# Performance work log

Measured on AMD Instinct MI355X. Metric: run time of the kernel, lower is better.

The kernel has to match this reference:

```python
import jax, jax.numpy as jnp
import numpy as np

D_MODEL = 1024
N_HEADS = 16
WINDOW = 64              # window_size
HEAD_DIM = D_MODEL // N_HEADS
HALF = WINDOW // 2
NWIN = WINDOW + 1        # half tokens each side + self
LN_EPS = 1e-5


def _layernorm(x, g, b):
    mu = jnp.mean(x, axis=-1, keepdims=True)
    var = jnp.var(x, axis=-1, keepdims=True)
    return (x - mu) * jax.lax.rsqrt(var + LN_EPS) * g + b


def _linear_attention(q, k, v):
    # feature map phi(x) = elu(x) + 1; O(n) attention over full d_model
    q = jax.nn.elu(q) + 1.0
    k = jax.nn.elu(k) + 1.0
    kv = jnp.einsum('bsd,bse->bde', k, v)          # [B, D, D]
    num = jnp.einsum('bsd,bde->bse', q, kv)        # [B, S, D]
    denom = jnp.einsum('bsd,bd->bs', q, k.sum(axis=1))
    return num / (denom[..., None] + 1e-6)


def _window_attention(q, k, v, rel_bias):
    # sliding window attention with relative position bias, banded via offset scan
    B, S, _ = q.shape
    qh = q.reshape(B, S, N_HEADS, HEAD_DIM).transpose(0, 2, 1, 3)  # [B,H,S,Dh]
    kh = k.reshape(B, S, N_HEADS, HEAD_DIM).transpose(0, 2, 1, 3)
    vh = v.reshape(B, S, N_HEADS, HEAD_DIM).transpose(0, 2, 1, 3)
    kp = jnp.pad(kh, ((0, 0), (0, 0), (HALF, HALF), (0, 0)))
    vp = jnp.pad(vh, ((0, 0), (0, 0), (HALF, HALF), (0, 0)))
    pos = jnp.arange(S)
    scale = np.float32(1.0 / np.sqrt(HEAD_DIM))

    def score_step(_, w):
        off = w - HALF                                   # relative offset in [-HALF, HALF]
        ks = jax.lax.dynamic_slice_in_dim(kp, w, S, axis=2)   # k at position i+off
        s = jnp.einsum('bhsd,bhsd->bhs', qh, ks) * scale
        s = s + rel_bias[off + WINDOW][None, :, None]    # bias per head for this offset
        valid = (pos + off >= 0) & (pos + off < S)
        s = jnp.where(valid[None, None, :], s, -jnp.inf)
        return None, s

    _, scores = jax.lax.scan(score_step, None, jnp.arange(NWIN))  # [W,B,H,S]
    attn = jax.nn.softmax(scores, axis=0)                          # softmax over window

    def out_step(acc, aw):
        a, w = aw
        vs = jax.lax.dynamic_slice_in_dim(vp, w, S, axis=2)
        return acc + a[..., None] * vs, None

    out, _ = jax.lax.scan(out_step, jnp.zeros_like(qh), (attn, jnp.arange(NWIN)))
    return out.transpose(0, 2, 1, 3).reshape(B, S, D_MODEL)


def setup_inputs() -> dict:
    key = jax.random.key(0)
    ks = jax.random.split(key, 16)

    def lin(k, fan_in, shape):
        return (jax.random.normal(k, shape, jnp.float32) / np.sqrt(fan_in)).astype(jnp.float32)

    D = D_MODEL
    inp = {
        'x': jax.random.normal(ks[0], (2, 2048, D), jnp.float32),
        'wq_lin': lin(ks[1], D, (D, D)), 'bq_lin': jnp.zeros((D,), jnp.float32),
        'wk_lin': lin(ks[2], D, (D, D)), 'bk_lin': jnp.zeros((D,), jnp.float32),
        'wv_lin': lin(ks[3], D, (D, D)), 'bv_lin': jnp.zeros((D,), jnp.float32),
        'wq_loc': lin(ks[4], D, (D, D)), 'bq_loc': jnp.zeros((D,), jnp.float32),
        'wk_loc': lin(ks[5], D, (D, D)), 'bk_loc': jnp.zeros((D,), jnp.float32),
        'wv_loc': lin(ks[6], D, (D, D)), 'bv_loc': jnp.zeros((D,), jnp.float32),
        'wo': lin(ks[7], D, (D, D)), 'bo': jnp.zeros((D,), jnp.float32),
        'wg1': lin(ks[8], 3 * D, (3 * D, D)), 'bg1': jnp.zeros((D,), jnp.float32),
        'wg2': lin(ks[9], D, (D, D)), 'bg2': jnp.zeros((D,), jnp.float32),
        'rel_bias': jax.random.normal(ks[10], (2 * WINDOW + 1, N_HEADS), jnp.float32),
        'ln_g': jnp.ones((D,), jnp.float32),
        'ln_b': jnp.zeros((D,), jnp.float32),
    }
    return inp


def reference(x, wq_lin, bq_lin, wk_lin, bk_lin, wv_lin, bv_lin,
              wq_loc, bq_loc, wk_loc, bk_loc, wv_loc, bv_loc,
              wo, bo, wg1, bg1, wg2, bg2, rel_bias, ln_g, ln_b):
    h = _layernorm(x, ln_g, ln_b)
    lin_out = _linear_attention(h @ wq_lin + bq_lin,
                                h @ wk_lin + bk_lin,
                                h @ wv_lin + bv_lin)
    win_out = _window_attention(h @ wq_loc + bq_loc,
                                h @ wk_loc + bk_loc,
                                h @ wv_loc + bv_loc, rel_bias)
    gate_in = jnp.concatenate([lin_out, win_out, h], axis=-1)
    gate = jax.nn.sigmoid(jnp.maximum(gate_in @ wg1 + bg1, 0.0) @ wg2 + bg2)
    out = gate * lin_out + (1.0 - gate) * win_out
    return out @ wo + bo + x
```

## Files before the change

kernel.cpp:

```cpp
#include <hip/hip_runtime.h>

typedef unsigned short u16;
typedef unsigned int u32;
typedef float f32x4 __attribute__((ext_vector_type(4)));
typedef __bf16 bf16x8 __attribute__((ext_vector_type(8)));

#define SEQ 2048
#define DM 1024

__device__ __forceinline__ float bf2f(u16 a){
  u32 b = ((u32)a) << 16; float f; __builtin_memcpy(&f, &b, 4); return f;
}
__device__ __forceinline__ u16 f2bf(float f){
  u32 b; __builtin_memcpy(&b, &f, 4);
  b += 0x7fffu + ((b >> 16) & 1u);
  return (u16)(b >> 16);
}

__device__ __forceinline__ void gload16(const void* g, void* l){
  __builtin_amdgcn_global_load_lds((const __attribute__((address_space(1))) u32*)g,
                                   (__attribute__((address_space(3))) u32*)l, 16, 0, 0);
}

#define SBAR  __builtin_amdgcn_sched_barrier(0); __builtin_amdgcn_s_barrier(); __builtin_amdgcn_sched_barrier(0);
#define VM0   asm volatile("s_waitcnt vmcnt(0)" ::: "memory"); __builtin_amdgcn_sched_barrier(0);
#define VM6   asm volatile("s_waitcnt vmcnt(6)" ::: "memory"); __builtin_amdgcn_sched_barrier(0);
#define VM8   asm volatile("s_waitcnt vmcnt(8)" ::: "memory"); __builtin_amdgcn_sched_barrier(0);

#define MFMA16(AF, BF) \
  __builtin_amdgcn_s_setprio(1); \
  _Pragma("unroll") for (int m_ = 0; m_ < 4; m_++) \
  _Pragma("unroll") for (int n_ = 0; n_ < 4; n_++) \
    acc[m_][n_] = __builtin_amdgcn_mfma_f32_16x16x32_bf16(AF[m_], BF[n_], acc[m_][n_], 0,0,0); \
  __builtin_amdgcn_s_setprio(0);

struct TP { const float* src[9]; u16* dst[9]; int K[9]; };

__global__ __launch_bounds__(256) void ktransall(TP tp){
  __shared__ float tile[64][65];
  int z = blockIdx.z;
  int K = tp.K[z];
  int kb = blockIdx.y << 6, nb = blockIdx.x << 6;
  if (kb >= K) return;
  const float* W = tp.src[z];
  u16* WT = tp.dst[z];
  const int N = 1024;
  int t = threadIdx.x;
  #pragma unroll
  for (int i = 0; i < 4; i++){
    int idx = t + (i << 8);
    int r = idx >> 4, c = (idx & 15) << 2;
    float4 v = *(const float4*)(W + (size_t)(kb + r) * N + nb + c);
    tile[r][c] = v.x; tile[r][c+1] = v.y; tile[r][c+2] = v.z; tile[r][c+3] = v.w;
  }
  __syncthreads();
  #pragma unroll
  for (int i = 0; i < 2; i++){
    int idx = t + (i << 8);
    int n = idx >> 3, k8 = (idx & 7) << 3;
    union { u16 s[8]; int4 v; } u;
    #pragma unroll
    for (int j = 0; j < 8; j++) u.s[j] = f2bf(tile[k8 + j][n]);
    *(int4*)(WT + (size_t)(nb + n) * K + kb + k8) = u.v;
  }
}

__global__ __launch_bounds__(256) void kln(const float* __restrict__ x, const float* __restrict__ gg,
                                           const float* __restrict__ bb, u16* __restrict__ h){
  int row = blockIdx.x, t = threadIdx.x;
  float4 xv = ((const float4*)(x + (size_t)row * DM))[t];
  float s  = xv.x + xv.y + xv.z + xv.w;
  float s2 = xv.x*xv.x + xv.y*xv.y + xv.z*xv.z + xv.w*xv.w;
  #pragma unroll
  for (int o = 1; o < 64; o <<= 1){ s += __shfl_xor(s, o); s2 += __shfl_xor(s2, o); }
  __shared__ float r1[4], r2[4];
  if ((t & 63) == 0){ r1[t >> 6] = s; r2[t >> 6] = s2; }
  __syncthreads();
  float S = r1[0]+r1[1]+r1[2]+r1[3], S2 = r2[0]+r2[1]+r2[2]+r2[3];
  float mu = S * (1.0f/DM);
  float var = S2 * (1.0f/DM) - mu*mu;
  float rstd = rsqrtf(var + 1e-5f);
  float4 gv = ((const float4*)gg)[t], bv = ((const float4*)bb)[t];
  ushort4 o;
  o.x = f2bf((xv.x - mu)*rstd*gv.x + bv.x);
  o.y = f2bf((xv.y - mu)*rstd*gv.y + bv.y);
  o.z = f2bf((xv.z - mu)*rstd*gv.z + bv.z);
  o.w = f2bf((xv.w - mu)*rstd*gv.w + bv.w);
  ((ushort4*)(h + (size_t)row * DM))[t] = o;
}

__device__ __forceinline__ float phi_elu(float v){ return v > 0.f ? v + 1.f : __expf(v); }

__global__ __launch_bounds__(512, 2) void kqkv8(
  const u16* __restrict__ h,
  const u16* wt0, const u16* wt1, const u16* wt2, const u16* wt3, const u16* wt4, const u16* wt5,
  const float* b0, const float* b1, const float* b2, const float* b3, const float* b4, const float* b5,
  u16* phiQ, u16* phiKT, u16* vT, u16* qloc, u16* kloc, u16* vloc)
{
  extern __shared__ char smem[];
  char* LA0 = smem;
  char* LA1 = smem + 16384;
  char* LB0 = smem + 32768;
  char* LB1 = smem + 65536;

  const int t = threadIdx.x, lane = t & 63, w = t >> 6;
  const int wm = w >> 2, wn = w & 3;

  int bid = blockIdx.x;
  int swz = (bid & 7) * 96 + (bid >> 3);
  int mt = swz & 31, ntile = swz >> 5;
  int m0 = mt << 7;
  int n0g = ntile << 8;
  int wi = n0g >> 10;
  int n0 = n0g & 1023;
  const u16* Bp = wi==0?wt0: wi==1?wt1: wi==2?wt2: wi==3?wt3: wi==4?wt4: wt5;
  const float* bsel = wi==0?b0: wi==1?b1: wi==2?b2: wi==3?b3: wi==4?b4: b5;

  auto stageA = [&](char* dst, int kt){
    #pragma unroll
    for (int j = 0; j < 2; j++){
      int slot = (j << 9) + t;
      int r = slot >> 3;
      int csw = ((slot & 7) << 4) ^ ((r & 7) << 4);
      gload16((const char*)(h + (size_t)(m0 + r) * 1024 + (kt << 6)) + csw,
              dst + (((j << 9) + (w << 6)) << 4));
    }
  };
  auto stageB = [&](char* dst, int kt){
    #pragma unroll
    for (int j = 0; j < 4; j++){
      int slot = (j << 9) + t;
      int r = slot >> 3;
      int csw = ((slot & 7) << 4) ^ ((r & 7) << 4);
      gload16((const char*)(Bp + (size_t)(n0 + r) * 1024 + (kt << 6)) + csw,
              dst + (((j << 9) + (w << 6)) << 4));
    }
  };
  auto rdA = [&](const char* ab, int m, int kk) -> bf16x8 {
    int ra = (wm << 6) + (m << 4) + (lane & 15);
    return *(const bf16x8*)(ab + (ra << 7) + (((kk << 6) + ((lane >> 4) << 4)) ^ ((ra & 7) << 4)));
  };
  auto rdB = [&](const char* bb, int n, int kk) -> bf16x8 {
    int rb = (wn << 6) + (n << 4) + (lane & 15);
    return *(const bf16x8*)(bb + (rb << 7) + (((kk << 6) + ((lane >> 4) << 4)) ^ ((rb & 7) << 4)));
  };

  f32x4 acc[4][4];
  #pragma unroll
  for (int m = 0; m < 4; m++)
    #pragma unroll
    for (int n = 0; n < 4; n++) acc[m][n] = (f32x4){0.f,0.f,0.f,0.f};

  const int NT = 16;
  bf16x8 a0[4], bq0[4], a1[4], bq1[4];

  stageA(LA0, 0); stageB(LB0, 0);
  stageA(LA1, 1); stageB(LB1, 1);
  VM6 SBAR
  #pragma unroll
  for (int m = 0; m < 4; m++) a0[m] = rdA(LA0, m, 0);
  #pragma unroll
  for (int n = 0; n < 4; n++) bq0[n] = rdB(LB0, n, 0);

  #pragma unroll 1
  for (int i = 0; i < NT/2; i++){
    int e = 2*i, o = e + 1;
    int se = (e + 2 < NT) ? e + 2 : NT - 1;
    int so = (o + 2 < NT) ? o + 2 : NT - 1;
    #pragma unroll
    for (int m = 0; m < 4; m++) a1[m] = rdA(LA0, m, 1);
    #pragma unroll
    for (int n = 0; n < 4; n++) bq1[n] = rdB(LB0, n, 1);
    SBAR
    stageA(LA0, se); stageB(LB0, se);
    MFMA16(a0, bq0)
    VM6 SBAR
    #pragma unroll
    for (int m = 0; m < 4; m++) a0[m] = rdA(LA1, m, 0);
    #pragma unroll
    for (int n = 0; n < 4; n++) bq0[n] = rdB(LB1, n, 0);
    MFMA16(a1, bq1)
    #pragma unroll
    for (int m = 0; m < 4; m++) a1[m] = rdA(LA1, m, 1);
    #pragma unroll
    for (int n = 0; n < 4; n++) bq1[n] = rdB(LB1, n, 1);
    SBAR
    stageA(LA1, so); stageB(LB1, so);
    MFMA16(a0, bq0)
    VM6 SBAR
    if (i < NT/2 - 1){
      #pragma unroll
      for (int m = 0; m < 4; m++) a0[m] = rdA(LA0, m, 0);
      #pragma unroll
      for (int n = 0; n < 4; n++) bq0[n] = rdB(LB0, n, 0);
    }
    MFMA16(a1, bq1)
  }
  VM0

  #pragma unroll
  for (int n = 0; n < 4; n++){
    int col = n0 + (wn << 6) + (n << 4) + (lane & 15);
    float bv = bsel[col];
    #pragma unroll
    for (int m = 0; m < 4; m++){
      int r0 = m0 + (wm << 6) + (m << 4) + ((lane >> 4) << 2);
      float e[4];
      #pragma unroll
      for (int r = 0; r < 4; r++) e[r] = acc[m][n][r] + bv;
      if (wi == 0){
        #pragma unroll
        for (int r = 0; r < 4; r++) phiQ[(size_t)(r0 + r) * DM + col] = f2bf(phi_elu(e[r]));
      } else if (wi == 1 || wi == 2){
        union { u16 s[4]; ushort4 v; } o;
        #pragma unroll
        for (int r = 0; r < 4; r++) o.s[r] = f2bf(wi == 1 ? phi_elu(e[r]) : e[r]);
        int bb = r0 >> 11, sl = r0 & 2047;
        u16* dst = (wi == 1) ? phiKT : vT;
        *(ushort4*)(dst + ((size_t)(bb << 10) + col) * SEQ + sl) = o.v;
      } else {
        u16* dst = wi==3 ? qloc : wi==4 ? kloc : vloc;
        #pragma unroll
        for (int r = 0; r < 4; r++) dst[(size_t)(r0 + r) * DM + col] = f2bf(e[r]);
      }
    }
  }
}

template<int NCHUNK>
__device__ __forceinline__ void pipe128(const u16* A0c, const u16* A1c, const u16* A2c, int lda,
                                        const u16* B, int ldb, int K, int m0, int n0,
                                        char* LA0, char* LA1, char* LB0, char* LB1,
                                        f32x4 (&acc)[4][4])
{
  const int t = threadIdx.x, lane = t & 63, w = t >> 6;
  const int wm = w >> 1, wn = w & 1;
  const int NT = K >> 6;

  auto stageA = [&](char* dst, int kt){
    const u16* Ab;
    if (NCHUNK == 3){
      int ci = kt >> 4;
      const u16* cp = (ci == 0) ? A0c : ((ci == 1) ? A1c : A2c);
      Ab = cp + ((kt & 15) << 6);
    } else {
      Ab = A0c + (kt << 6);
    }
    #pragma unroll
    for (int j = 0; j < 4; j++){
      int slot = (j << 8) + t;
      int r = slot >> 3;
      int csw = ((slot & 7) << 4) ^ ((r & 7) << 4);
// ... 48 lines not shown
    for (int m = 0; m < 4; m++) a0[m] = rdA(LA1, m, 0);
    #pragma unroll
    for (int n = 0; n < 4; n++) bq0[n] = rdB(LB1, n, 0);
    MFMA16(a1, bq1)
    #pragma unroll
    for (int m = 0; m < 4; m++) a1[m] = rdA(LA1, m, 1);
    #pragma unroll
    for (int n = 0; n < 4; n++) bq1[n] = rdB(LB1, n, 1);
    SBAR
    stageA(LA1, so); stageB(LB1, so);
    MFMA16(a0, bq0)
    VM8 SBAR
    if (i < NT/2 - 1){
      #pragma unroll
      for (int m = 0; m < 4; m++) a0[m] = rdA(LA0, m, 0);
      #pragma unroll
      for (int n = 0; n < 4; n++) bq0[n] = rdB(LB0, n, 0);
    }
    MFMA16(a1, bq1)
  }
  VM0
}

#define PIPE_LDS \
  __shared__ char LA0[16384], LA1[16384], LB0[16384], LB1[16384];

#define EPI_COORDS \
  const int lane = threadIdx.x & 63, w = threadIdx.x >> 6; \
  const int wm = w >> 1, wn = w & 1;

#define ZERO_ACC f32x4 acc[4][4]; \
  _Pragma("unroll") for (int m = 0; m < 4; m++) _Pragma("unroll") for (int n = 0; n < 4; n++) acc[m][n] = (f32x4){0.f,0.f,0.f,0.f};

__global__ __launch_bounds__(256) void kkv(const u16* __restrict__ vT, const u16* __restrict__ phiKT,
                                           u16* __restrict__ kvT){
  PIPE_LDS
  int b = blockIdx.z;
  int m0 = blockIdx.x << 7, n0 = blockIdx.y << 7;
  const u16* A = vT + (size_t)b * DM * SEQ;
  const u16* B = phiKT + (size_t)b * DM * SEQ;
  ZERO_ACC
  pipe128<1>(A, 0, 0, SEQ, B, SEQ, SEQ, m0, n0, LA0, LA1, LB0, LB1, acc);
  EPI_COORDS
  u16* C = kvT + (size_t)b * DM * DM;
  #pragma unroll
  for (int n = 0; n < 4; n++){
    int col = n0 + wn*64 + n*16 + (lane & 15);
    #pragma unroll
    for (int m = 0; m < 4; m++){
      int r0 = m0 + wm*64 + m*16 + ((lane >> 4) << 2);
      #pragma unroll
      for (int r = 0; r < 4; r++) C[(size_t)(r0 + r) * DM + col] = f2bf(acc[m][n][r]);
    }
  }
}

__global__ __launch_bounds__(256) void knum(const u16* __restrict__ phiQ, const u16* __restrict__ kvT,
                                            const float* __restrict__ dn, u16* __restrict__ lin){
  PIPE_LDS
  int b = blockIdx.z;
  int m0 = blockIdx.x << 7, n0 = blockIdx.y << 7;
  const u16* A = phiQ + (size_t)b * SEQ * DM;
  const u16* B = kvT + (size_t)b * DM * DM;
  ZERO_ACC
  pipe128<1>(A, 0, 0, DM, B, DM, DM, m0, n0, LA0, LA1, LB0, LB1, acc);
  EPI_COORDS
  #pragma unroll
  for (int n = 0; n < 4; n++){
    int col = n0 + wn*64 + n*16 + (lane & 15);
    #pragma unroll
    for (int m = 0; m < 4; m++){
      int r0 = m0 + wm*64 + m*16 + ((lane >> 4) << 2);
      #pragma unroll
      for (int r = 0; r < 4; r++){
        float d = dn[(b << 11) + r0 + r] + 1e-6f;
        lin[((size_t)(b << 11) + r0 + r) * DM + col] = f2bf(acc[m][n][r] / d);
      }
    }
  }
}

__global__ __launch_bounds__(256) void ksumk(const u16* __restrict__ kt, float* __restrict__ ks){
  int row = blockIdx.x, t = threadIdx.x;
  const ushort4* src = (const ushort4*)(kt + (size_t)row * SEQ);
  float s = 0.f;
  for (int i = t; i < 512; i += 256){
    ushort4 v = src[i];
    s += bf2f(v.x) + bf2f(v.y) + bf2f(v.z) + bf2f(v.w);
  }
  #pragma unroll
  for (int o = 1; o < 64; o <<= 1) s += __shfl_xor(s, o);
  __shared__ float red[4];
  if ((t & 63) == 0) red[t >> 6] = s;
  __syncthreads();
  if (t == 0) ks[row] = red[0] + red[1] + red[2] + red[3];
}

__global__ __launch_bounds__(256) void kdenom(const u16* __restrict__ phiQ, const float* __restrict__ ks,
                                              float* __restrict__ dn){
  int row = blockIdx.x, t = threadIdx.x;
  ushort4 v = ((const ushort4*)(phiQ + (size_t)row * DM))[t];
  float4 kk = ((const float4*)(ks + ((size_t)(row >> 11) << 10)))[t];
  float s = bf2f(v.x)*kk.x + bf2f(v.y)*kk.y + bf2f(v.z)*kk.z + bf2f(v.w)*kk.w;
  #pragma unroll
  for (int o = 1; o < 64; o <<= 1) s += __shfl_xor(s, o);
  __shared__ float red[4];
  if ((t & 63) == 0) red[t >> 6] = s;
  __syncthreads();
  if (t == 0) dn[row] = red[0] + red[1] + red[2] + red[3];
}

__global__ __launch_bounds__(256) void kwin(const u16* __restrict__ qloc, const u16* __restrict__ kloc,
                                            const u16* __restrict__ vloc, const float* __restrict__ rel_bias,
                                            u16* __restrict__ wout)
{
  __shared__ float KV[128 * 68];
  __shared__ float Ssm[64 * 84];
  __shared__ float bias_s[65];
  int qt = blockIdx.x, hh = blockIdx.y, b = blockIdx.z;
  int q0 = qt << 6;
  int t = threadIdx.x;
  int q = t >> 2, sub = t & 3, qq = q & 15;
  size_t base = (size_t)b * SEQ * DM + hh * 64;
  for (int i = t; i < 1024; i += 256){
    int r = i >> 3, seg = i & 7;
    int p = q0 + r - 32;
    float* dst = &KV[r * 68 + (seg << 3)];
    if ((unsigned)p < SEQ){
      int4 raw = *(const int4*)(kloc + base + (size_t)p * DM + (seg << 3));
      const u16* s = (const u16*)&raw;
      #pragma unroll
      for (int j = 0; j < 8; j++) dst[j] = bf2f(s[j]);
    } else {
      #pragma unroll
      for (int j = 0; j < 8; j++) dst[j] = 0.f;
    }
  }
  if (t < 65) bias_s[t] = rel_bias[(t + 32) * 16 + hh];
  float qreg[16];
  {
    const u16* qp = qloc + base + (size_t)(q0 + q) * DM + (sub << 4);
    int4 raw0 = *(const int4*)qp;
    int4 raw1 = *(const int4*)(qp + 8);
    const u16* s0 = (const u16*)&raw0; const u16* s1 = (const u16*)&raw1;
    #pragma unroll
    for (int j = 0; j < 8; j++){ qreg[j] = bf2f(s0[j]); qreg[8 + j] = bf2f(s1[j]); }
  }
  __syncthreads();
  int rlo = (t >> 6) << 4;
  for (int rr = 0; rr < 80; rr++){
    int r = rlo + rr;
    const float* kr = &KV[r * 68 + (sub << 4)];
    float s = 0.f;
    #pragma unroll
    for (int i = 0; i < 16; i++) s += qreg[i] * kr[i];
    s += __shfl_xor(s, 1); s += __shfl_xor(s, 2);
    int wrel = r - q;
    int p = q0 + r - 32;
    float sc = -1e30f;
    if ((unsigned)wrel <= 64u && (unsigned)p < SEQ) sc = s * 0.125f + bias_s[wrel];
    if (sub == 0) Ssm[q * 84 + rr] = sc;
  }
  __syncthreads();
  for (int i = t; i < 1024; i += 256){
    int r = i >> 3, seg = i & 7;
    int p = q0 + r - 32;
    float* dst = &KV[r * 68 + (seg << 3)];
    if ((unsigned)p < SEQ){
      int4 raw = *(const int4*)(vloc + base + (size_t)p * DM + (seg << 3));
      const u16* s = (const u16*)&raw;
      #pragma unroll
      for (int j = 0; j < 8; j++) dst[j] = bf2f(s[j]);
    } else {
      #pragma unroll
      for (int j = 0; j < 8; j++) dst[j] = 0.f;
    }
  }
  float mloc = -1e30f;
  for (int wrel = sub; wrel <= 64; wrel += 4) mloc = fmaxf(mloc, Ssm[q * 84 + qq + wrel]);
  mloc = fmaxf(mloc, __shfl_xor(mloc, 1));
  mloc = fmaxf(mloc, __shfl_xor(mloc, 2));
  float lloc = 0.f;
  for (int wrel = sub; wrel <= 64; wrel += 4) lloc += __expf(Ssm[q * 84 + qq + wrel] - mloc);
  lloc += __shfl_xor(lloc, 1); lloc += __shfl_xor(lloc, 2);
  float inv = 1.0f / lloc;
  for (int wrel = sub; wrel <= 64; wrel += 4)
    Ssm[q * 84 + qq + wrel] = __expf(Ssm[q * 84 + qq + wrel] - mloc) * inv;
  __syncthreads();
  float accv[16];
  #pragma unroll
  for (int i = 0; i < 16; i++) accv[i] = 0.f;
  for (int rr = 0; rr < 80; rr++){
    int r = rlo + rr;
    float pv = Ssm[q * 84 + rr];
    pv = ((unsigned)(r - q) <= 64u) ? pv : 0.f;
    const float* vr = &KV[r * 68 + (sub << 4)];
    #pragma unroll
    for (int i = 0; i < 16; i++) accv[i] += pv * vr[i];
  }
  union { u16 s[16]; int4 v[2]; } ob;
  #pragma unroll
  for (int i = 0; i < 16; i++) ob.s[i] = f2bf(accv[i]);
  u16* dst = wout + base + (size_t)(q0 + q) * DM + (sub << 4);
  *(int4*)dst = ob.v[0];
  *(int4*)(dst + 8) = ob.v[1];
}

__global__ __launch_bounds__(256) void kgate1(const u16* __restrict__ lin, const u16* __restrict__ win,
                                              const u16* __restrict__ h, const u16* __restrict__ wg1T,
                                              const float* __restrict__ bg1, u16* __restrict__ g1){
  PIPE_LDS
  int m0 = blockIdx.x << 7, n0 = blockIdx.y << 7;
  ZERO_ACC
  pipe128<3>(lin, win, h, DM, wg1T, 3072, 3072, m0, n0, LA0, LA1, LB0, LB1, acc);
  EPI_COORDS
  #pragma unroll
  for (int n = 0; n < 4; n++){
    int col = n0 + wn*64 + n*16 + (lane & 15);
    float bv = bg1[col];
    #pragma unroll
    for (int m = 0; m < 4; m++){
      int r0 = m0 + wm*64 + m*16 + ((lane >> 4) << 2);
      #pragma unroll
      for (int r = 0; r < 4; r++){
        float v = acc[m][n][r] + bv;
        g1[(size_t)(r0 + r) * DM + col] = f2bf(v > 0.f ? v : 0.f);
      }
    }
  }
}

__global__ __launch_bounds__(256) void kgate2(const u16* __restrict__ g1, const u16* __restrict__ wg2T,
                                              const float* __restrict__ bg2, const u16* __restrict__ lin,
                                              const u16* __restrict__ win, u16* __restrict__ outc){
  PIPE_LDS
  int m0 = blockIdx.x << 7, n0 = blockIdx.y << 7;
  ZERO_ACC
  pipe128<1>(g1, 0, 0, DM, wg2T, DM, DM, m0, n0, LA0, LA1, LB0, LB1, acc);
// ... 48 lines not shown
  const float* wq_lin = (const float*)d_in[1];  const float* bq_lin = (const float*)d_in[2];
  const float* wk_lin = (const float*)d_in[3];  const float* bk_lin = (const float*)d_in[4];
  const float* wv_lin = (const float*)d_in[5];  const float* bv_lin = (const float*)d_in[6];
  const float* wq_loc = (const float*)d_in[7];  const float* bq_loc = (const float*)d_in[8];
  const float* wk_loc = (const float*)d_in[9];  const float* bk_loc = (const float*)d_in[10];
  const float* wv_loc = (const float*)d_in[11]; const float* bv_loc = (const float*)d_in[12];
  const float* wo     = (const float*)d_in[13]; const float* bo     = (const float*)d_in[14];
  const float* wg1    = (const float*)d_in[15]; const float* bg1    = (const float*)d_in[16];
  const float* wg2    = (const float*)d_in[17]; const float* bg2    = (const float*)d_in[18];
  const float* rel_bias = (const float*)d_in[19];
  const float* ln_g   = (const float*)d_in[20]; const float* ln_b   = (const float*)d_in[21];

  char* ws = (char*)d_ws;
  size_t off = 0;
  auto alloc = [&](size_t bytes) -> void* {
    void* p = ws + off;
    off += (bytes + 255) & ~(size_t)255;
    return p;
  };
  const size_t MB2 = (size_t)1024 * 1024 * 2;
  const size_t ACT = (size_t)4096 * 1024 * 2;
  u16* wT[6]; for (int i = 0; i < 6; i++) wT[i] = (u16*)alloc(MB2);
  u16* woT   = (u16*)alloc(MB2);
  u16* wg1T  = (u16*)alloc((size_t)1024 * 3072 * 2);
  u16* wg2T  = (u16*)alloc(MB2);
  u16* hbf   = (u16*)alloc(ACT);
  u16* phiQ  = (u16*)alloc(ACT);
  u16* phiKT = (u16*)alloc(ACT);
  u16* vT    = (u16*)alloc(ACT);
  u16* qloc  = (u16*)alloc(ACT);
  u16* kloc  = (u16*)alloc(ACT);
  u16* vloc  = (u16*)alloc(ACT);
  u16* kvT   = (u16*)alloc(2 * MB2);
  float* ksum = (float*)alloc(2 * 1024 * 4);
  float* dnm  = (float*)alloc(4096 * 4);
  u16* lin   = (u16*)alloc(ACT);
  u16* win   = (u16*)alloc(ACT);
  u16* g1    = phiQ;
  u16* outc  = vT;

  hipFuncSetAttribute((const void*)kqkv8, hipFuncAttributeMaxDynamicSharedMemorySize, 98304);

  dim3 blk(256);
  TP tp;
  tp.src[0]=wq_lin; tp.src[1]=wk_lin; tp.src[2]=wv_lin; tp.src[3]=wq_loc; tp.src[4]=wk_loc;
  tp.src[5]=wv_loc; tp.src[6]=wo; tp.src[7]=wg1; tp.src[8]=wg2;
  tp.dst[0]=wT[0]; tp.dst[1]=wT[1]; tp.dst[2]=wT[2]; tp.dst[3]=wT[3]; tp.dst[4]=wT[4];
  tp.dst[5]=wT[5]; tp.dst[6]=woT; tp.dst[7]=wg1T; tp.dst[8]=wg2T;
  for (int i = 0; i < 9; i++) tp.K[i] = (i == 7) ? 3072 : 1024;
  ktransall<<<dim3(16,48,9), blk, 0, stream>>>(tp);

  kln<<<4096, blk, 0, stream>>>(x, ln_g, ln_b, hbf);

  kqkv8<<<768, 512, 98304, stream>>>(hbf, wT[0], wT[1], wT[2], wT[3], wT[4], wT[5],
                                     bq_lin, bk_lin, bv_lin, bq_loc, bk_loc, bv_loc,
                                     phiQ, phiKT, vT, qloc, kloc, vloc);

  ksumk<<<2048, blk, 0, stream>>>(phiKT, ksum);
  kdenom<<<4096, blk, 0, stream>>>(phiQ, ksum, dnm);
  kkv<<<dim3(8,8,2), blk, 0, stream>>>(vT, phiKT, kvT);
  knum<<<dim3(16,8,2), blk, 0, stream>>>(phiQ, kvT, dnm, lin);

  kwin<<<dim3(32,16,2), blk, 0, stream>>>(qloc, kloc, vloc, rel_bias, win);

  kgate1<<<dim3(32,8), blk, 0, stream>>>(lin, win, hbf, wg1T, bg1, g1);
  kgate2<<<dim3(32,8), blk, 0, stream>>>(g1, wg2T, bg2, lin, win, outc);
  kfinal<<<dim3(32,8), blk, 0, stream>>>(outc, woT, bo, x, (float*)d_out);
}
```

Before: 264.4 us.

## Enlarge QKV projection GEMM tile to 256x256 with 4 waves per block

The fused six-way QKV projection kernel moves from 128x256 tiles with 8 waves (2 blocks per CU) to 256x256 tiles with 4 waves, each wave computing a 128x128 sub-tile with an 8x8 MFMA accumulator grid. The aim is more operand reuse per LDS read and less global traffic per FLOP. The cost is heavy register pressure from 64 accumulator vectors plus fragments, only one block per CU, 128 KB of LDS, and just 384 blocks on the GPU. The wait counts are updated to match the larger number of loads per stage.

```diff
diff --git a/kernel.cpp b/kernel.cpp
--- a/kernel.cpp
+++ b/kernel.cpp
@@ -24,13 +24,20 @@
 
 #define SBAR  __builtin_amdgcn_sched_barrier(0); __builtin_amdgcn_s_barrier(); __builtin_amdgcn_sched_barrier(0);
 #define VM0   asm volatile("s_waitcnt vmcnt(0)" ::: "memory"); __builtin_amdgcn_sched_barrier(0);
-#define VM6   asm volatile("s_waitcnt vmcnt(6)" ::: "memory"); __builtin_amdgcn_sched_barrier(0);
 #define VM8   asm volatile("s_waitcnt vmcnt(8)" ::: "memory"); __builtin_amdgcn_sched_barrier(0);
+#define VM16  asm volatile("s_waitcnt vmcnt(16)" ::: "memory"); __builtin_amdgcn_sched_barrier(0);
 
 #define MFMA16(AF, BF) \
   __builtin_amdgcn_s_setprio(1); \
   _Pragma("unroll") for (int m_ = 0; m_ < 4; m_++) \
   _Pragma("unroll") for (int n_ = 0; n_ < 4; n_++) \
+    acc[m_][n_] = __builtin_amdgcn_mfma_f32_16x16x32_bf16(AF[m_], BF[n_], acc[m_][n_], 0,0,0); \
+  __builtin_amdgcn_s_setprio(0);
+
+#define MFMA64(AF, BF) \
+  __builtin_amdgcn_s_setprio(1); \
+  _Pragma("unroll") for (int m_ = 0; m_ < 8; m_++) \
+  _Pragma("unroll") for (int n_ = 0; n_ < 8; n_++) \
     acc[m_][n_] = __builtin_amdgcn_mfma_f32_16x16x32_bf16(AF[m_], BF[n_], acc[m_][n_], 0,0,0); \
   __builtin_amdgcn_s_setprio(0);
 
@@ -91,7 +98,7 @@
 
 __device__ __forceinline__ float phi_elu(float v){ return v > 0.f ? v + 1.f : __expf(v); }
 
-__global__ __launch_bounds__(512, 2) void kqkv8(
+__global__ __launch_bounds__(256, 1) void kqkvF(
   const u16* __restrict__ h,
   const u16* wt0, const u16* wt1, const u16* wt2, const u16* wt3, const u16* wt4, const u16* wt5,
   const float* b0, const float* b1, const float* b2, const float* b3, const float* b4, const float* b5,
@@ -99,17 +106,17 @@
 {
   extern __shared__ char smem[];
   char* LA0 = smem;
-  char* LA1 = smem + 16384;
-  char* LB0 = smem + 32768;
-  char* LB1 = smem + 65536;
+  char* LA1 = smem + 32768;
+  char* LB0 = smem + 65536;
+  char* LB1 = smem + 98304;
 
   const int t = threadIdx.x, lane = t & 63, w = t >> 6;
-  const int wm = w >> 2, wn = w & 3;
+  const int wm = w >> 1, wn = w & 1;
 
   int bid = blockIdx.x;
-  int swz = (bid & 7) * 96 + (bid >> 3);
-  int mt = swz & 31, ntile = swz >> 5;
-  int m0 = mt << 7;
+  int swz = (bid & 7) * 48 + (bid >> 3);
+  int mt = swz & 15, ntile = swz >> 4;
+  int m0 = mt << 8;
   int n0g = ntile << 8;
   int wi = n0g >> 10;
   int n0 = n0g & 1023;
@@ -118,93 +125,92 @@
 
   auto stageA = [&](char* dst, int kt){
     #pragma unroll
-    for (int j = 0; j < 2; j++){
-      int slot = (j << 9) + t;
+    for (int j = 0; j < 8; j++){
+      int slot = (j << 8) + t;
       int r = slot >> 3;
       int csw = ((slot & 7) << 4) ^ ((r & 7) << 4);
       gload16((const char*)(h + (size_t)(m0 + r) * 1024 + (kt << 6)) + csw,
-              dst + (((j << 9) + (w << 6)) << 4));
+              dst + (((j << 8) + (w << 6)) << 4));
     }
   };
   auto stageB = [&](char* dst, int kt){
     #pragma unroll
-    for (int j = 0; j < 4; j++){
-      int slot = (j << 9) + t;
+    for (int j = 0; j < 8; j++){
+      int slot = (j << 8) + t;
       int r = slot >> 3;
       int csw = ((slot & 7) << 4) ^ ((r & 7) << 4);
       gload16((const char*)(Bp + (size_t)(n0 + r) * 1024 + (kt << 6)) + csw,
-              dst + (((j << 9) + (w << 6)) << 4));
+              dst + (((j << 8) + (w << 6)) << 4));
     }
   };
   auto rdA = [&](const char* ab, int m, int kk) -> bf16x8 {
-    int ra = (wm << 6) + (m << 4) + (lane & 15);
+    int ra = (wm << 7) + (m << 4) + (lane & 15);
     return *(const bf16x8*)(ab + (ra << 7) + (((kk << 6) + ((lane >> 4) << 4)) ^ ((ra & 7) << 4)));
   };
   auto rdB = [&](const char* bb, int n, int kk) -> bf16x8 {
-    int rb = (wn << 6) + (n << 4) + (lane & 15);
+    int rb = (wn << 7) + (n << 4) + (lane & 15);
     return *(const bf16x8*)(bb + (rb << 7) + (((kk << 6) + ((lane >> 4) << 4)) ^ ((rb & 7) << 4)));
   };
 
-  f32x4 acc[4][4];
-  #pragma unroll
-  for (int m = 0; m < 4; m++)
-    #pragma unroll
-    for (int n = 0; n < 4; n++) acc[m][n] = (f32x4){0.f,0.f,0.f,0.f};
-
-  const int NT = 16;
-  bf16x8 a0[4], bq0[4], a1[4], bq1[4];
+  f32x4 acc[8][8];
+  #pragma unroll
+  for (int m = 0; m < 8; m++)
+    #pragma unroll
+    for (int n = 0; n < 8; n++) acc[m][n] = (f32x4){0.f,0.f,0.f,0.f};
+
+  bf16x8 a0[8], b0f[8], a1[8], b1f[8];
 
   stageA(LA0, 0); stageB(LB0, 0);
   stageA(LA1, 1); stageB(LB1, 1);
-  VM6 SBAR
-  #pragma unroll
-  for (int m = 0; m < 4; m++) a0[m] = rdA(LA0, m, 0);
-  #pragma unroll
-  for (int n = 0; n < 4; n++) bq0[n] = rdB(LB0, n, 0);
+  VM16 SBAR
+  #pragma unroll
+  for (int m = 0; m < 8; m++) a0[m] = rdA(LA0, m, 0);
+  #pragma unroll
+  for (int n = 0; n < 8; n++) b0f[n] = rdB(LB0, n, 0);
 
   #pragma unroll 1
-  for (int i = 0; i < NT/2; i++){
+  for (int i = 0; i < 8; i++){
     int e = 2*i, o = e + 1;
-    int se = (e + 2 < NT) ? e + 2 : NT - 1;
-    int so = (o + 2 < NT) ? o + 2 : NT - 1;
-    #pragma unroll
-    for (int m = 0; m < 4; m++) a1[m] = rdA(LA0, m, 1);
-    #pragma unroll
-    for (int n = 0; n < 4; n++) bq1[n] = rdB(LB0, n, 1);
+    int se = (e + 2 < 16) ? e + 2 : 15;
+    int so = (o + 2 < 16) ? o + 2 : 15;
+    #pragma unroll
+    for (int m = 0; m < 8; m++) a1[m] = rdA(LA0, m, 1);
+    #pragma unroll
+    for (int n = 0; n < 8; n++) b1f[n] = rdB(LB0, n, 1);
     SBAR
     stageA(LA0, se); stageB(LB0, se);
-    MFMA16(a0, bq0)
-    VM6 SBAR
-    #pragma unroll
-    for (int m = 0; m < 4; m++) a0[m] = rdA(LA1, m, 0);
-    #pragma unroll
-    for (int n = 0; n < 4; n++) bq0[n] = rdB(LB1, n, 0);
-    MFMA16(a1, bq1)
-    #pragma unroll
-    for (int m = 0; m < 4; m++) a1[m] = rdA(LA1, m, 1);
-    #pragma unroll
-    for (int n = 0; n < 4; n++) bq1[n] = rdB(LB1, n, 1);
+    MFMA64(a0, b0f)
+    VM16 SBAR
+    #pragma unroll
+    for (int m = 0; m < 8; m++) a0[m] = rdA(LA1, m, 0);
+    #pragma unroll
+    for (int n = 0; n < 8; n++) b0f[n] = rdB(LB1, n, 0);
+    MFMA64(a1, b1f)
+    #pragma unroll
+    for (int m = 0; m < 8; m++) a1[m] = rdA(LA1, m, 1);
+    #pragma unroll
+    for (int n = 0; n < 8; n++) b1f[n] = rdB(LB1, n, 1);
     SBAR
     stageA(LA1, so); stageB(LB1, so);
-    MFMA16(a0, bq0)
-    VM6 SBAR
-    if (i < NT/2 - 1){
-      #pragma unroll
-      for (int m = 0; m < 4; m++) a0[m] = rdA(LA0, m, 0);
-      #pragma unroll
-      for (int n = 0; n < 4; n++) bq0[n] = rdB(LB0, n, 0);
-    }
-    MFMA16(a1, bq1)
+    MFMA64(a0, b0f)
+    VM16 SBAR
+    if (i < 7){
+      #pragma unroll
+      for (int m = 0; m < 8; m++) a0[m] = rdA(LA0, m, 0);
+      #pragma unroll
+      for (int n = 0; n < 8; n++) b0f[n] = rdB(LB0, n, 0);
+    }
+    MFMA64(a1, b1f)
   }
   VM0
 
   #pragma unroll
-  for (int n = 0; n < 4; n++){
-    int col = n0 + (wn << 6) + (n << 4) + (lane & 15);
+  for (int n = 0; n < 8; n++){
+    int col = n0 + (wn << 7) + (n << 4) + (lane & 15);
     float bv = bsel[col];
     #pragma unroll
-    for (int m = 0; m < 4; m++){
-      int r0 = m0 + (wm << 6) + (m << 4) + ((lane >> 4) << 2);
+    for (int m = 0; m < 8; m++){
+      int r0 = m0 + (wm << 7) + (m << 4) + ((lane >> 4) << 2);
       float e[4];
       #pragma unroll
       for (int r = 0; r < 4; r++) e[r] = acc[m][n][r] + bv;
@@ -212,12 +218,12 @@
         #pragma unroll
         for (int r = 0; r < 4; r++) phiQ[(size_t)(r0 + r) * DM + col] = f2bf(phi_elu(e[r]));
       } else if (wi == 1 || wi == 2){
-        union { u16 s[4]; ushort4 v; } o;
+        union { u16 s[4]; ushort4 v; } ov;
         #pragma unroll
-        for (int r = 0; r < 4; r++) o.s[r] = f2bf(wi == 1 ? phi_elu(e[r]) : e[r]);
+        for (int r = 0; r < 4; r++) ov.s[r] = f2bf(wi == 1 ? phi_elu(e[r]) : e[r]);
         int bb = r0 >> 11, sl = r0 & 2047;
         u16* dst = (wi == 1) ? phiKT : vT;
-        *(ushort4*)(dst + ((size_t)(bb << 10) + col) * SEQ + sl) = o.v;
+        *(ushort4*)(dst + ((size_t)(bb << 10) + col) * SEQ + sl) = ov.v;
       } else {
         u16* dst = wi==3 ? qloc : wi==4 ? kloc : vloc;
         #pragma unroll
@@ -625,7 +631,7 @@
   u16* g1    = phiQ;
   u16* outc  = vT;
 
-  hipFuncSetAttribute((const void*)kqkv8, hipFuncAttributeMaxDynamicSharedMemorySize, 98304);
+  hipFuncSetAttribute((const void*)kqkvF, hipFuncAttributeMaxDynamicSharedMemorySize, 131072);
 
   dim3 blk(256);
   TP tp;
@@ -638,9 +644,9 @@
 
   kln<<<4096, blk, 0, stream>>>(x, ln_g, ln_b, hbf);
 
-  kqkv8<<<768, 512, 98304, stream>>>(hbf, wT[0], wT[1], wT[2], wT[3], wT[4], wT[5],
-                                     bq_lin, bk_lin, bv_lin, bq_loc, bk_loc, bv_loc,
-                                     phiQ, phiKT, vT, qloc, kloc, vloc);
+  kqkvF<<<384, 256, 131072, stream>>>(hbf, wT[0], wT[1], wT[2], wT[3], wT[4], wT[5],
+                                      bq_lin, bk_lin, bv_lin, bq_loc, bk_loc, bv_loc,
+                                      phiQ, phiKT, vT, qloc, kloc, vloc);
 
   ksumk<<<2048, blk, 0, stream>>>(phiKT, ksum);
   kdenom<<<4096, blk, 0, stream>>>(phiQ, ksum, dnm);
```

Result: slower. 470.3 us (+77.9%).

## Switch QKV GEMM to triple-buffered LDS pipeline with simpler per-tile loop

Applied to the files above, without the earlier changes.

Restructures the fused QKV projection GEMM from a double-buffered, 2x-unrolled software pipeline with register-level fragment prefetch to a triple-buffered LDS ring (48KB per stage, 144KB total). Each iteration loads fragments, issues the prefetch two tiles ahead, and waits on LDS before each MFMA group. The aim is more latency tolerance for global loads. The cost is that the block now uses 144KB of LDS and launch bounds drop to one block per CU, which lowers occupancy and removes the overlap of LDS reads with MFMAs that the old code had.

```diff
diff --git a/kernel.cpp b/kernel.cpp
--- a/kernel.cpp
+++ b/kernel.cpp
@@ -23,6 +23,7 @@
 }
 
 #define SBAR  __builtin_amdgcn_sched_barrier(0); __builtin_amdgcn_s_barrier(); __builtin_amdgcn_sched_barrier(0);
+#define LGKM0 asm volatile("s_waitcnt lgkmcnt(0)" ::: "memory"); __builtin_amdgcn_sched_barrier(0);
 #define VM0   asm volatile("s_waitcnt vmcnt(0)" ::: "memory"); __builtin_amdgcn_sched_barrier(0);
 #define VM6   asm volatile("s_waitcnt vmcnt(6)" ::: "memory"); __builtin_amdgcn_sched_barrier(0);
 #define VM8   asm volatile("s_waitcnt vmcnt(8)" ::: "memory"); __builtin_amdgcn_sched_barrier(0);
@@ -91,18 +92,13 @@
 
 __device__ __forceinline__ float phi_elu(float v){ return v > 0.f ? v + 1.f : __expf(v); }
 
-__global__ __launch_bounds__(512, 2) void kqkv8(
+__global__ __launch_bounds__(512, 1) void kqkv9(
   const u16* __restrict__ h,
   const u16* wt0, const u16* wt1, const u16* wt2, const u16* wt3, const u16* wt4, const u16* wt5,
   const float* b0, const float* b1, const float* b2, const float* b3, const float* b4, const float* b5,
   u16* phiQ, u16* phiKT, u16* vT, u16* qloc, u16* kloc, u16* vloc)
 {
   extern __shared__ char smem[];
-  char* LA0 = smem;
-  char* LA1 = smem + 16384;
-  char* LB0 = smem + 32768;
-  char* LB1 = smem + 65536;
-
   const int t = threadIdx.x, lane = t & 63, w = t >> 6;
   const int wm = w >> 2, wn = w & 3;
 
@@ -136,11 +132,18 @@
               dst + (((j << 9) + (w << 6)) << 4));
     }
   };
-  auto rdA = [&](const char* ab, int m, int kk) -> bf16x8 {
+  auto stageTile = [&](int buf, int kt){
+    char* base = smem + buf * 49152;
+    stageA(base, kt);
+    stageB(base + 16384, kt);
+  };
+  auto rdA = [&](int buf, int m, int kk) -> bf16x8 {
+    const char* ab = smem + buf * 49152;
     int ra = (wm << 6) + (m << 4) + (lane & 15);
     return *(const bf16x8*)(ab + (ra << 7) + (((kk << 6) + ((lane >> 4) << 4)) ^ ((ra & 7) << 4)));
   };
-  auto rdB = [&](const char* bb, int n, int kk) -> bf16x8 {
+  auto rdB = [&](int buf, int n, int kk) -> bf16x8 {
+    const char* bb = smem + buf * 49152 + 16384;
     int rb = (wn << 6) + (n << 4) + (lane & 15);
     return *(const bf16x8*)(bb + (rb << 7) + (((kk << 6) + ((lane >> 4) << 4)) ^ ((rb & 7) << 4)));
   };
@@ -152,49 +155,33 @@
     for (int n = 0; n < 4; n++) acc[m][n] = (f32x4){0.f,0.f,0.f,0.f};
 
   const int NT = 16;
-  bf16x8 a0[4], bq0[4], a1[4], bq1[4];
-
-  stageA(LA0, 0); stageB(LB0, 0);
-  stageA(LA1, 1); stageB(LB1, 1);
-  VM6 SBAR
-  #pragma unroll
-  for (int m = 0; m < 4; m++) a0[m] = rdA(LA0, m, 0);
-  #pragma unroll
-  for (int n = 0; n < 4; n++) bq0[n] = rdB(LB0, n, 0);
+  stageTile(0, 0);
+  stageTile(1, 1);
+  VM6
+  SBAR
 
   #pragma unroll 1
-  for (int i = 0; i < NT/2; i++){
-    int e = 2*i, o = e + 1;
-    int se = (e + 2 < NT) ? e + 2 : NT - 1;
-    int so = (o + 2 < NT) ? o + 2 : NT - 1;
-    #pragma unroll
-    for (int m = 0; m < 4; m++) a1[m] = rdA(LA0, m, 1);
-    #pragma unroll
-    for (int n = 0; n < 4; n++) bq1[n] = rdB(LB0, n, 1);
+  for (int tt = 0; tt < NT; tt++){
+    int buf = tt % 3;
+    int st = (tt + 2 < NT) ? tt + 2 : NT - 1;
+    int sbuf = (tt + 2) % 3;
+    bf16x8 af[4], bf[4];
+    #pragma unroll
+    for (int m = 0; m < 4; m++) af[m] = rdA(buf, m, 0);
+    #pragma unroll
+    for (int n = 0; n < 4; n++) bf[n] = rdB(buf, n, 0);
     SBAR
-    stageA(LA0, se); stageB(LB0, se);
-    MFMA16(a0, bq0)
-    VM6 SBAR
-    #pragma unroll
-    for (int m = 0; m < 4; m++) a0[m] = rdA(LA1, m, 0);
-    #pragma unroll
-    for (int n = 0; n < 4; n++) bq0[n] = rdB(LB1, n, 0);
-    MFMA16(a1, bq1)
-    #pragma unroll
-    for (int m = 0; m < 4; m++) a1[m] = rdA(LA1, m, 1);
-    #pragma unroll
-    for (int n = 0; n < 4; n++) bq1[n] = rdB(LB1, n, 1);
+    stageTile(sbuf, st);
+    LGKM0
+    MFMA16(af, bf)
+    #pragma unroll
+    for (int m = 0; m < 4; m++) af[m] = rdA(buf, m, 1);
+    #pragma unroll
+    for (int n = 0; n < 4; n++) bf[n] = rdB(buf, n, 1);
+    VM6
     SBAR
-    stageA(LA1, so); stageB(LB1, so);
-    MFMA16(a0, bq0)
-    VM6 SBAR
-    if (i < NT/2 - 1){
-      #pragma unroll
-      for (int m = 0; m < 4; m++) a0[m] = rdA(LA0, m, 0);
-      #pragma unroll
-      for (int n = 0; n < 4; n++) bq0[n] = rdB(LB0, n, 0);
-    }
-    MFMA16(a1, bq1)
+    LGKM0
+    MFMA16(af, bf)
   }
   VM0
 
@@ -625,7 +612,7 @@
   u16* g1    = phiQ;
   u16* outc  = vT;
 
-  hipFuncSetAttribute((const void*)kqkv8, hipFuncAttributeMaxDynamicSharedMemorySize, 98304);
+  hipFuncSetAttribute((const void*)kqkv9, hipFuncAttributeMaxDynamicSharedMemorySize, 147456);
 
   dim3 blk(256);
   TP tp;
@@ -638,9 +625,9 @@
 
   kln<<<4096, blk, 0, stream>>>(x, ln_g, ln_b, hbf);
 
-  kqkv8<<<768, 512, 98304, stream>>>(hbf, wT[0], wT[1], wT[2], wT[3], wT[4], wT[5],
-                                     bq_lin, bk_lin, bv_lin, bq_loc, bk_loc, bv_loc,
-                                     phiQ, phiKT, vT, qloc, kloc, vloc);
+  kqkv9<<<768, 512, 147456, stream>>>(hbf, wT[0], wT[1], wT[2], wT[3], wT[4], wT[5],
+                                      bq_lin, bk_lin, bv_lin, bq_loc, bk_loc, bv_loc,
+                                      phiQ, phiKT, vT, qloc, kloc, vloc);
 
   ksumk<<<2048, blk, 0, stream>>>(phiKT, ksum);
   kdenom<<<4096, blk, 0, stream>>>(phiQ, ksum, dnm);
```

Result: no change. 265.1 us (+0.3%).

## Fuse split-K kv GEMM with window attention into one launch

Applied to the files above, without the earlier changes.

The kv GEMM is split along the sequence dimension into two halves, giving 256 tiles instead of 128. It is merged with the window-attention kernel into a single heterogeneous launch, with block index choosing the role and shared memory dynamic, so the two independent workloads share the GPU. A small kernel then sums the two bf16 partial kv products. This aims to fix underutilisation of the 128-block kv GEMM and remove launch serialisation. In exchange it adds an extra pass over the partials and rounds each partial to bf16 before summing.

```diff
diff --git a/kernel.cpp b/kernel.cpp
--- a/kernel.cpp
+++ b/kernel.cpp
@@ -332,27 +332,140 @@
 #define ZERO_ACC f32x4 acc[4][4]; \
   _Pragma("unroll") for (int m = 0; m < 4; m++) _Pragma("unroll") for (int n = 0; n < 4; n++) acc[m][n] = (f32x4){0.f,0.f,0.f,0.f};
 
-__global__ __launch_bounds__(256) void kkv(const u16* __restrict__ vT, const u16* __restrict__ phiKT,
-                                           u16* __restrict__ kvT){
-  PIPE_LDS
-  int b = blockIdx.z;
-  int m0 = blockIdx.x << 7, n0 = blockIdx.y << 7;
-  const u16* A = vT + (size_t)b * DM * SEQ;
-  const u16* B = phiKT + (size_t)b * DM * SEQ;
-  ZERO_ACC
-  pipe128<1>(A, 0, 0, SEQ, B, SEQ, SEQ, m0, n0, LA0, LA1, LB0, LB1, acc);
-  EPI_COORDS
-  u16* C = kvT + (size_t)b * DM * DM;
-  #pragma unroll
-  for (int n = 0; n < 4; n++){
-    int col = n0 + wn*64 + n*16 + (lane & 15);
-    #pragma unroll
-    for (int m = 0; m < 4; m++){
-      int r0 = m0 + wm*64 + m*16 + ((lane >> 4) << 2);
-      #pragma unroll
-      for (int r = 0; r < 4; r++) C[(size_t)(r0 + r) * DM + col] = f2bf(acc[m][n][r]);
-    }
-  }
+__global__ __launch_bounds__(256) void kkvwin(
+  const u16* __restrict__ vT, const u16* __restrict__ phiKT,
+  u16* __restrict__ kvp0, u16* __restrict__ kvp1,
+  const u16* __restrict__ qloc, const u16* __restrict__ kloc,
+  const u16* __restrict__ vloc, const float* __restrict__ rel_bias,
+  u16* __restrict__ wout)
+{
+  extern __shared__ char sm[];
+  int bid = blockIdx.x;
+  int t = threadIdx.x;
+  if (bid < 256){
+    int mt = bid & 7, nt = (bid >> 3) & 7, b = (bid >> 6) & 1, kh = bid >> 7;
+    int m0 = mt << 7, n0 = nt << 7;
+    const u16* A = vT + (size_t)b * DM * SEQ + (kh << 10);
+    const u16* B = phiKT + (size_t)b * DM * SEQ + (kh << 10);
+    char* LA0 = sm; char* LA1 = sm + 16384; char* LB0 = sm + 32768; char* LB1 = sm + 49152;
+    ZERO_ACC
+    pipe128<1>(A, 0, 0, SEQ, B, SEQ, 1024, m0, n0, LA0, LA1, LB0, LB1, acc);
+    EPI_COORDS
+    u16* C = (kh ? kvp1 : kvp0) + (size_t)b * DM * DM;
+    #pragma unroll
+    for (int n = 0; n < 4; n++){
+      int col = n0 + wn*64 + n*16 + (lane & 15);
+      #pragma unroll
+      for (int m = 0; m < 4; m++){
+        int r0 = m0 + wm*64 + m*16 + ((lane >> 4) << 2);
+        #pragma unroll
+        for (int r = 0; r < 4; r++) C[(size_t)(r0 + r) * DM + col] = f2bf(acc[m][n][r]);
+      }
+    }
+  } else {
+    int i = bid - 256;
+    int qt = i & 31, hh = (i >> 5) & 15, b = i >> 9;
+    float* KV = (float*)sm;
+    float* Ssm = (float*)(sm + 34816);
+    float* bias_s = (float*)(sm + 56320);
+    int q0 = qt << 6;
+    int q = t >> 2, sub = t & 3, qq = q & 15;
+    size_t base = (size_t)b * SEQ * DM + hh * 64;
+    for (int ii = t; ii < 1024; ii += 256){
+      int r = ii >> 3, seg = ii & 7;
+      int p = q0 + r - 32;
+      float* dst = &KV[r * 68 + (seg << 3)];
+      if ((unsigned)p < SEQ){
+        int4 raw = *(const int4*)(kloc + base + (size_t)p * DM + (seg << 3));
+        const u16* s = (const u16*)&raw;
+        #pragma unroll
+        for (int j = 0; j < 8; j++) dst[j] = bf2f(s[j]);
+      } else {
+        #pragma unroll
+        for (int j = 0; j < 8; j++) dst[j] = 0.f;
+      }
+    }
+    if (t < 65) bias_s[t] = rel_bias[(t + 32) * 16 + hh];
+    float qreg[16];
+    {
+      const u16* qp = qloc + base + (size_t)(q0 + q) * DM + (sub << 4);
+      int4 raw0 = *(const int4*)qp;
+      int4 raw1 = *(const int4*)(qp + 8);
+      const u16* s0 = (const u16*)&raw0; const u16* s1 = (const u16*)&raw1;
+      #pragma unroll
+      for (int j = 0; j < 8; j++){ qreg[j] = bf2f(s0[j]); qreg[8 + j] = bf2f(s1[j]); }
+    }
+    __syncthreads();
+    int rlo = (t >> 6) << 4;
+    for (int rr = 0; rr < 80; rr++){
+      int r = rlo + rr;
+      const float* kr = &KV[r * 68 + (sub << 4)];
+      float s = 0.f;
+      #pragma unroll
+      for (int ii = 0; ii < 16; ii++) s += qreg[ii] * kr[ii];
+      s += __shfl_xor(s, 1); s += __shfl_xor(s, 2);
+      int wrel = r - q;
+      int p = q0 + r - 32;
+      float sc = -1e30f;
+      if ((unsigned)wrel <= 64u && (unsigned)p < SEQ) sc = s * 0.125f + bias_s[wrel];
+      if (sub == 0) Ssm[q * 84 + rr] = sc;
+    }
+    __syncthreads();
+    for (int ii = t; ii < 1024; ii += 256){
+      int r = ii >> 3, seg = ii & 7;
+      int p = q0 + r - 32;
+      float* dst = &KV[r * 68 + (seg << 3)];
+      if ((unsigned)p < SEQ){
+        int4 raw = *(const int4*)(vloc + base + (size_t)p * DM + (seg << 3));
+        const u16* s = (const u16*)&raw;
+        #pragma unroll
+        for (int j = 0; j < 8; j++) dst[j] = bf2f(s[j]);
+      } else {
+        #pragma unroll
+        for (int j = 0; j < 8; j++) dst[j] = 0.f;
+      }
+    }
+    float mloc = -1e30f;
+    for (int wrel = sub; wrel <= 64; wrel += 4) mloc = fmaxf(mloc, Ssm[q * 84 + qq + wrel]);
+    mloc = fmaxf(mloc, __shfl_xor(mloc, 1));
+    mloc = fmaxf(mloc, __shfl_xor(mloc, 2));
+    float lloc = 0.f;
+    for (int wrel = sub; wrel <= 64; wrel += 4) lloc += __expf(Ssm[q * 84 + qq + wrel] - mloc);
+    lloc += __shfl_xor(lloc, 1); lloc += __shfl_xor(lloc, 2);
+    float inv = 1.0f / lloc;
+    for (int wrel = sub; wrel <= 64; wrel += 4)
+      Ssm[q * 84 + qq + wrel] = __expf(Ssm[q * 84 + qq + wrel] - mloc) * inv;
+    __syncthreads();
+    float accv[16];
+    #pragma unroll
+    for (int ii = 0; ii < 16; ii++) accv[ii] = 0.f;
+    for (int rr = 0; rr < 80; rr++){
+      int r = rlo + rr;
+      float pv = Ssm[q * 84 + rr];
+      pv = ((unsigned)(r - q) <= 64u) ? pv : 0.f;
+      const float* vr = &KV[r * 68 + (sub << 4)];
+      #pragma unroll
+      for (int ii = 0; ii < 16; ii++) accv[ii] += pv * vr[ii];
+    }
+    union { u16 s[16]; int4 v[2]; } ob;
+    #pragma unroll
+    for (int ii = 0; ii < 16; ii++) ob.s[ii] = f2bf(accv[ii]);
+    u16* dst = wout + base + (size_t)(q0 + q) * DM + (sub << 4);
+    *(int4*)dst = ob.v[0];
+    *(int4*)(dst + 8) = ob.v[1];
+  }
+}
+
+__global__ __launch_bounds__(256) void kvadd(const u16* __restrict__ a, const u16* __restrict__ bsrc,
+                                             u16* __restrict__ c){
+  size_t i = ((size_t)blockIdx.x * 256 + threadIdx.x) * 8;
+  int4 ra = *(const int4*)(a + i);
+  int4 rb = *(const int4*)(bsrc + i);
+  const u16* pa = (const u16*)&ra; const u16* pb = (const u16*)&rb;
+  union { u16 s[8]; int4 v; } o;
+  #pragma unroll
+  for (int j = 0; j < 8; j++) o.s[j] = f2bf(bf2f(pa[j]) + bf2f(pb[j]));
+  *(int4*)(c + i) = o.v;
 }
 
 __global__ __launch_bounds__(256) void knum(const u16* __restrict__ phiQ, const u16* __restrict__ kvT,
@@ -408,102 +521,6 @@
   if ((t & 63) == 0) red[t >> 6] = s;
   __syncthreads();
   if (t == 0) dn[row] = red[0] + red[1] + red[2] + red[3];
-}
-
-__global__ __launch_bounds__(256) void kwin(const u16* __restrict__ qloc, const u16* __restrict__ kloc,
-                                            const u16* __restrict__ vloc, const float* __restrict__ rel_bias,
-                                            u16* __restrict__ wout)
-{
-  __shared__ float KV[128 * 68];
-  __shared__ float Ssm[64 * 84];
-  __shared__ float bias_s[65];
-  int qt = blockIdx.x, hh = blockIdx.y, b = blockIdx.z;
-  int q0 = qt << 6;
-  int t = threadIdx.x;
-  int q = t >> 2, sub = t & 3, qq = q & 15;
-  size_t base = (size_t)b * SEQ * DM + hh * 64;
-  for (int i = t; i < 1024; i += 256){
-    int r = i >> 3, seg = i & 7;
-    int p = q0 + r - 32;
-    float* dst = &KV[r * 68 + (seg << 3)];
-    if ((unsigned)p < SEQ){
-      int4 raw = *(const int4*)(kloc + base + (size_t)p * DM + (seg << 3));
-      const u16* s = (const u16*)&raw;
-      #pragma unroll
-      for (int j = 0; j < 8; j++) dst[j] = bf2f(s[j]);
-    } else {
-      #pragma unroll
-      for (int j = 0; j < 8; j++) dst[j] = 0.f;
-    }
-  }
-  if (t < 65) bias_s[t] = rel_bias[(t + 32) * 16 + hh];
-  float qreg[16];
-  {
-    const u16* qp = qloc + base + (size_t)(q0 + q) * DM + (sub << 4);
-    int4 raw0 = *(const int4*)qp;
-    int4 raw1 = *(const int4*)(qp + 8);
-    const u16* s0 = (const u16*)&raw0; const u16* s1 = (const u16*)&raw1;
-    #pragma unroll
-    for (int j = 0; j < 8; j++){ qreg[j] = bf2f(s0[j]); qreg[8 + j] = bf2f(s1[j]); }
-  }
-  __syncthreads();
-  int rlo = (t >> 6) << 4;
-  for (int rr = 0; rr < 80; rr++){
-    int r = rlo + rr;
-    const float* kr = &KV[r * 68 + (sub << 4)];
-    float s = 0.f;
-    #pragma unroll
-    for (int i = 0; i < 16; i++) s += qreg[i] * kr[i];
-    s += __shfl_xor(s, 1); s += __shfl_xor(s, 2);
-    int wrel = r - q;
-    int p = q0 + r - 32;
-    float sc = -1e30f;
-    if ((unsigned)wrel <= 64u && (unsigned)p < SEQ) sc = s * 0.125f + bias_s[wrel];
-    if (sub == 0) Ssm[q * 84 + rr] = sc;
-  }
-  __syncthreads();
-  for (int i = t; i < 1024; i += 256){
-    int r = i >> 3, seg = i & 7;
-    int p = q0 + r - 32;
-    float* dst = &KV[r * 68 + (seg << 3)];
-    if ((unsigned)p < SEQ){
-      int4 raw = *(const int4*)(vloc + base + (size_t)p * DM + (seg << 3));
-      const u16* s = (const u16*)&raw;
-      #pragma unroll
-      for (int j = 0; j < 8; j++) dst[j] = bf2f(s[j]);
-    } else {
-      #pragma unroll
-      for (int j = 0; j < 8; j++) dst[j] = 0.f;
-    }
-  }
-  float mloc = -1e30f;
-  for (int wrel = sub; wrel <= 64; wrel += 4) mloc = fmaxf(mloc, Ssm[q * 84 + qq + wrel]);
-  mloc = fmaxf(mloc, __shfl_xor(mloc, 1));
-  mloc = fmaxf(mloc, __shfl_xor(mloc, 2));
-  float lloc = 0.f;
-  for (int wrel = sub; wrel <= 64; wrel += 4) lloc += __expf(Ssm[q * 84 + qq + wrel] - mloc);
-  lloc += __shfl_xor(lloc, 1); lloc += __shfl_xor(lloc, 2);
-  float inv = 1.0f / lloc;
-  for (int wrel = sub; wrel <= 64; wrel += 4)
-    Ssm[q * 84 + qq + wrel] = __expf(Ssm[q * 84 + qq + wrel] - mloc) * inv;
-  __syncthreads();
-  float accv[16];
-  #pragma unroll
-  for (int i = 0; i < 16; i++) accv[i] = 0.f;
-  for (int rr = 0; rr < 80; rr++){
-    int r = rlo + rr;
-    float pv = Ssm[q * 84 + rr];
-    pv = ((unsigned)(r - q) <= 64u) ? pv : 0.f;
-    const float* vr = &KV[r * 68 + (sub << 4)];
-    #pragma unroll
-    for (int i = 0; i < 16; i++) accv[i] += pv * vr[i];
-  }
-  union { u16 s[16]; int4 v[2]; } ob;
-  #pragma unroll
-  for (int i = 0; i < 16; i++) ob.s[i] = f2bf(accv[i]);
-  u16* dst = wout + base + (size_t)(q0 + q) * DM + (sub << 4);
-  *(int4*)dst = ob.v[0];
-  *(int4*)(dst + 8) = ob.v[1];
 }
 
 __global__ __launch_bounds__(256) void kgate1(const u16* __restrict__ lin, const u16* __restrict__ win,
@@ -618,6 +635,8 @@
   u16* kloc  = (u16*)alloc(ACT);
   u16* vloc  = (u16*)alloc(ACT);
   u16* kvT   = (u16*)alloc(2 * MB2);
+  u16* kvp0  = (u16*)alloc(2 * MB2);
+  u16* kvp1  = (u16*)alloc(2 * MB2);
   float* ksum = (float*)alloc(2 * 1024 * 4);
   float* dnm  = (float*)alloc(4096 * 4);
   u16* lin   = (u16*)alloc(ACT);
@@ -626,6 +645,7 @@
   u16* outc  = vT;
 
   hipFuncSetAttribute((const void*)kqkv8, hipFuncAttributeMaxDynamicSharedMemorySize, 98304);
+  hipFuncSetAttribute((const void*)kkvwin, hipFuncAttributeMaxDynamicSharedMemorySize, 65536);
 
   dim3 blk(256);
   TP tp;
@@ -644,10 +664,11 @@
 
   ksumk<<<2048, blk, 0, stream>>>(phiKT, ksum);
   kdenom<<<4096, blk, 0, stream>>>(phiQ, ksum, dnm);
-  kkv<<<dim3(8,8,2), blk, 0, stream>>>(vT, phiKT, kvT);
+
+  kkvwin<<<1280, blk, 65536, stream>>>(vT, phiKT, kvp0, kvp1, qloc, kloc, vloc, rel_bias, win);
+  kvadd<<<1024, blk, 0, stream>>>(kvp0, kvp1, kvT);
+
   knum<<<dim3(16,8,2), blk, 0, stream>>>(phiQ, kvT, dnm, lin);
-
-  kwin<<<dim3(32,16,2), blk, 0, stream>>>(qloc, kloc, vloc, rel_bias, win);
 
   kgate1<<<dim3(32,8), blk, 0, stream>>>(lin, win, hbf, wg1T, bg1, g1);
   kgate2<<<dim3(32,8), blk, 0, stream>>>(g1, wg2T, bg2, lin, win, outc);
```

Result: slower. 295.1 us (+11.6%).
